# Kernel optimization log

Hardware: AMD Instinct MI355X
Metric: run time of the kernel (lower is better)

The kernel has to match this reference:

```python
import jax, jax.numpy as jnp
import numpy as np

POOLED_H = 7
POOLED_W = 7
SPATIAL_SCALE = 0.0625
B, C, H, W = 8, 256, 48, 48
R = 300
IMG = 768  # = H / SPATIAL_SCALE


def setup_inputs() -> dict:
    key = jax.random.key(0)
    k1, k2, k3, k4 = jax.random.split(key, 4)
    features = jax.random.normal(k1, (B, C, H, W), dtype=jnp.float32)
    # rois: (batch_idx, x1, y1, x2, y2) in input-image coords
    bidx = jax.random.randint(k2, (R, 1), 0, B).astype(jnp.float32)
    tl = jax.random.uniform(k3, (R, 2), minval=0.0, maxval=IMG - 64.0)
    wh = jax.random.uniform(k4, (R, 2), minval=32.0, maxval=320.0)
    br = jnp.minimum(tl + wh, IMG - 1.0)
    rois = jnp.concatenate([bidx, tl, br], axis=1).astype(jnp.float32)
    return {"features": features, "rois": rois}


def _hat_integral(x, grid):
    """Integral from -inf to x of the unit hat basis function centered at each
    grid point g (support [g-1, g+1], peak 1, total mass 1).
    x: [..., 1-broadcastable], grid: [G] -> returns [..., G]."""
    t = x[..., None] - (grid - 1.0)
    return jnp.where(
        t <= 0.0, 0.0,
        jnp.where(t <= 1.0, 0.5 * t * t,
                  jnp.where(t <= 2.0, 1.0 - 0.5 * (2.0 - t) ** 2, 1.0)))


def reference(features, rois):
    # Precise RoI Pooling: exact double integral of the bilinear interpolant
    # over each bin, divided by bin area. Bilinear interp (with zero padding
    # outside the map, as in the CUDA PrRoIPoolingGetData) is
    #   f(u,v) = sum_{j,i} feat[j,i] * hat_j(v) * hat_i(u)
    # so the bin integral factorizes into per-axis hat-integral weights.
    Bf, Cf, Hf, Wf = features.shape
    bidx = rois[:, 0].astype(jnp.int32)
    x1 = rois[:, 1] * SPATIAL_SCALE
    y1 = rois[:, 2] * SPATIAL_SCALE
    x2 = rois[:, 3] * SPATIAL_SCALE
    y2 = rois[:, 4] * SPATIAL_SCALE
    roi_w = jnp.maximum(x2 - x1, 0.0)
    roi_h = jnp.maximum(y2 - y1, 0.0)
    bin_w = roi_w / POOLED_W  # [R]
    bin_h = roi_h / POOLED_H

    ph = jnp.arange(POOLED_H, dtype=jnp.float32)
    pw = jnp.arange(POOLED_W, dtype=jnp.float32)
    ya = y1[:, None] + ph[None, :] * bin_h[:, None]  # [R, PH]
    yb = ya + bin_h[:, None]
    xa = x1[:, None] + pw[None, :] * bin_w[:, None]  # [R, PW]
    xb = xa + bin_w[:, None]

    gy = jnp.arange(Hf, dtype=jnp.float32)
    gx = jnp.arange(Wf, dtype=jnp.float32)
    Wy = _hat_integral(yb, gy) - _hat_integral(ya, gy)  # [R, PH, H]
    Wx = _hat_integral(xb, gx) - _hat_integral(xa, gx)  # [R, PW, W]

    feat = features[bidx]  # [R, C, H, W]
    t = jnp.einsum('rpj,rcji->rcpi', Wy, feat)   # integrate over y
    num = jnp.einsum('rqi,rcpi->rcpq', Wx, t)    # integrate over x -> [R,C,PH,PW]

    area = (bin_w * bin_h)[:, None, None, None]  # win_size per ROI
    out = jnp.where(area > 0.0, num / jnp.where(area > 0.0, area, 1.0), 0.0)
    return out
```

## Files before the change

kernel.cpp:

```cpp
#include <hip/hip_runtime.h>


#define PH 7
#define PW 7
#define NBINS 49
#define SCALE 0.0625f
#define CH 256
#define FH 48
#define FW 48
#define RNUM 300
#define CB 8
#define MAXJ 23
#define ROWF 28

__device__ __forceinline__ float hat_int(float x, float g) {
    float t = x - (g - 1.0f);
    if (t <= 0.0f) return 0.0f;
    if (t <= 1.0f) return 0.5f * t * t;
    if (t <= 2.0f) { float u = 2.0f - t; return 1.0f - 0.5f * u * u; }
    return 1.0f;
}

__global__ __launch_bounds__(256)
void prroi_fused(const float* __restrict__ feat,
                 const float* __restrict__ rois,
                 float* __restrict__ out) {
    const int cblk = blockIdx.x;
    const int r    = blockIdx.y;
    const int c0   = cblk * CB;
    const int tid  = threadIdx.x;

    __shared__ float patch[CB * MAXJ * ROWF];
    __shared__ float s_wy[PH][6];
    __shared__ float s_wx[PW][6];
    __shared__ int   s_jb[PH], s_jc[PH];
    __shared__ int   s_ib[PW], s_ic[PW];

    const float* roi = rois + r * 5;
    const int   b  = (int)roi[0];
    const float x1 = roi[1] * SCALE, y1 = roi[2] * SCALE;
    const float x2 = roi[3] * SCALE, y2 = roi[4] * SCALE;
    const float roi_w = fmaxf(x2 - x1, 0.0f), roi_h = fmaxf(y2 - y1, 0.0f);
    const float bin_w = roi_w / (float)PW, bin_h = roi_h / (float)PH;
    const float area = bin_w * bin_h;
    const float inv_area = (area > 0.0f) ? (1.0f / area) : 0.0f;

    const float ylo = fminf(y1, y2), yhi = fmaxf(y1, y2);
    const float xlo = fminf(x1, x2), xhi = fmaxf(x1, x2);
    const int j0  = max(0, (int)floorf(ylo) - 1);
    const int j1  = min(FH - 1, (int)floorf(yhi) + 1);
    const int i0  = max(0, (int)floorf(xlo) - 1);
    const int i1  = min(FW - 1, (int)floorf(xhi) + 1);
    const int i0a = i0 & ~3;
    const int jspan = j1 - j0 + 1;
    const int ni4   = ((i1 - i0a) >> 2) + 1;

    if (tid < PH + PW) {
        if (tid < PH) {
            const int ph = tid;
            const float ya = y1 + ph * bin_h, yb = ya + bin_h;
            int jb0 = max(0, (int)floorf(ya) - 1);
            int jb1 = min(FH - 1, (int)floorf(yb) + 1);
            jb0 = max(jb0, j0); jb1 = min(jb1, j1);
            s_jb[ph] = jb0 - j0;
            s_jc[ph] = jb1 - jb0 + 1;
#pragma unroll
            for (int k = 0; k < 6; ++k) {
                const float g = (float)(jb0 + k);
                s_wy[ph][k] = hat_int(yb, g) - hat_int(ya, g);
            }
        } else {
            const int pw = tid - PH;
            const float xa = x1 + pw * bin_w, xb = xa + bin_w;
            int ib0 = max(0, (int)floorf(xa) - 1);
            int ib1 = min(FW - 1, (int)floorf(xb) + 1);
            ib0 = max(ib0, i0); ib1 = min(ib1, i1);
            s_ib[pw] = ib0 - i0a;
            s_ic[pw] = ib1 - ib0 + 1;
#pragma unroll
            for (int k = 0; k < 6; ++k) {
                const float g = (float)(ib0 + k);
                s_wx[pw][k] = hat_int(xb, g) - hat_int(xa, g);
            }
        }
    }

    const int per_c  = jspan * ni4;
    const int total  = CB * per_c;
    const float* fb  = feat + (size_t)(b * CH + c0) * FH * FW;
    for (int idx = tid; idx < total; idx += 256) {
        const int c  = idx / per_c;
        const int rj = idx - c * per_c;
        const int j  = rj / ni4;
        const int i4 = rj - j * ni4;
        const float4 v = *(const float4*)(fb + ((size_t)c * FH + (j0 + j)) * FW + i0a + 4 * i4);
        *(float4*)(&patch[(c * MAXJ + j) * ROWF + 4 * i4]) = v;
    }
    __syncthreads();

    const int lane = tid & 63;
    const int wv   = tid >> 6;
    if (lane < NBINS) {
        const int ph = lane / PW;
        const int pw = lane - ph * PW;
        const int jb = s_jb[ph], jc = s_jc[ph];
        const int ib = s_ib[pw], ic = s_ic[pw];
#pragma unroll
        for (int p = 0; p < 2; ++p) {
            const int c = p * 4 + wv;
            const float* pc = &patch[(c * MAXJ + jb) * ROWF + ib];
            float acc = 0.0f;
            for (int jj = 0; jj < jc; ++jj) {
                const float wy = s_wy[ph][jj];
                const float* prow = pc + jj * ROWF;
                float rs = 0.0f;
                for (int ii = 0; ii < ic; ++ii)
                    rs += s_wx[pw][ii] * prow[ii];
                acc += wy * rs;
            }
            out[((size_t)r * CH + c0 + c) * NBINS + lane] = acc * inv_area;
        }
    }
}

extern "C" void kernel_launch(void* const* d_in, const int* in_sizes, int n_in,
                              void* d_out, int out_size, void* d_ws, size_t ws_size,
                              hipStream_t stream) {
    const float* feat = (const float*)d_in[0];
    const float* rois = (const float*)d_in[1];
    float* out = (float*)d_out;

    prroi_fused<<<dim3(CH / CB, RNUM), 256, 0, stream>>>(feat, rois, out);
}
```

Before: 106.3 us.

## Transpose patch to channel-innermost layout and vectorize bin accumulation over channels

Doubles channels per block to 16 and stores the shared-memory patch with channels innermost, transposing four channels at a time during the load. Each thread now handles one bin and four channels, reading float4 across channels and holding the y/x weights in registers, with the inner x loop unrolled. This cuts shared-memory load instructions and weight reloads and halves the block count. The cost is a larger shared footprint, which may lower occupancy, and more lanes left idle (196 of 256 active).

Result: faster. 99.14 us (-6.7%).

```diff
diff --git a/kernel.cpp b/kernel.cpp
--- a/kernel.cpp
+++ b/kernel.cpp
@@ -9,7 +9,7 @@
 #define FH 48
 #define FW 48
 #define RNUM 300
-#define CB 8
+#define CB 16
 #define MAXJ 23
 #define ROWF 28
 
@@ -30,7 +30,7 @@
     const int c0   = cblk * CB;
     const int tid  = threadIdx.x;
 
-    __shared__ float patch[CB * MAXJ * ROWF];
+    __shared__ float patch[MAXJ * ROWF * CB];
     __shared__ float s_wy[PH][6];
     __shared__ float s_wx[PW][6];
     __shared__ int   s_jb[PH], s_jc[PH];
@@ -85,41 +85,62 @@
         }
     }
 
-    const int per_c  = jspan * ni4;
-    const int total  = CB * per_c;
-    const float* fb  = feat + (size_t)(b * CH + c0) * FH * FW;
-    for (int idx = tid; idx < total; idx += 256) {
-        const int c  = idx / per_c;
-        const int rj = idx - c * per_c;
-        const int j  = rj / ni4;
-        const int i4 = rj - j * ni4;
-        const float4 v = *(const float4*)(fb + ((size_t)c * FH + (j0 + j)) * FW + i0a + 4 * i4);
-        *(float4*)(&patch[(c * MAXJ + j) * ROWF + 4 * i4]) = v;
+    const float* fb = feat + (size_t)(b * CH + c0) * FH * FW;
+    for (int u = tid; u < 4 * MAXJ * 7; u += 256) {
+        const int q   = u / (MAXJ * 7);
+        const int rem = u - q * (MAXJ * 7);
+        const int j   = rem / 7;
+        const int i4  = rem - j * 7;
+        if (j < jspan && i4 < ni4) {
+            int ig = i0a + 4 * i4;
+            if (ig > FW - 4) ig = FW - 4;
+            const float* src = fb + ((size_t)(4 * q) * FH + (j0 + j)) * FW + ig;
+            const float4 v0 = *(const float4*)(src);
+            const float4 v1 = *(const float4*)(src + FH * FW);
+            const float4 v2 = *(const float4*)(src + 2 * FH * FW);
+            const float4 v3 = *(const float4*)(src + 3 * FH * FW);
+            float* dst = &patch[((size_t)j * ROWF + (ig - i0a)) * CB + 4 * q];
+            *(float4*)(dst + 0 * CB) = make_float4(v0.x, v1.x, v2.x, v3.x);
+            *(float4*)(dst + 1 * CB) = make_float4(v0.y, v1.y, v2.y, v3.y);
+            *(float4*)(dst + 2 * CB) = make_float4(v0.z, v1.z, v2.z, v3.z);
+            *(float4*)(dst + 3 * CB) = make_float4(v0.w, v1.w, v2.w, v3.w);
+        }
     }
     __syncthreads();
 
-    const int lane = tid & 63;
-    const int wv   = tid >> 6;
-    if (lane < NBINS) {
-        const int ph = lane / PW;
-        const int pw = lane - ph * PW;
+    const int bin = tid >> 2;
+    const int q   = tid & 3;
+    if (bin < NBINS) {
+        const int ph = bin / PW;
+        const int pw = bin - ph * PW;
         const int jb = s_jb[ph], jc = s_jc[ph];
         const int ib = s_ib[pw], ic = s_ic[pw];
+        float wy[6], wx[6];
 #pragma unroll
-        for (int p = 0; p < 2; ++p) {
-            const int c = p * 4 + wv;
-            const float* pc = &patch[(c * MAXJ + jb) * ROWF + ib];
-            float acc = 0.0f;
-            for (int jj = 0; jj < jc; ++jj) {
-                const float wy = s_wy[ph][jj];
-                const float* prow = pc + jj * ROWF;
-                float rs = 0.0f;
-                for (int ii = 0; ii < ic; ++ii)
-                    rs += s_wx[pw][ii] * prow[ii];
-                acc += wy * rs;
+        for (int k = 0; k < 6; ++k) { wy[k] = s_wy[ph][k]; wx[k] = s_wx[pw][k]; }
+
+        float ax = 0.0f, ay = 0.0f, az = 0.0f, aw = 0.0f;
+        const float* pc = &patch[((size_t)jb * ROWF + ib) * CB + 4 * q];
+        for (int jj = 0; jj < jc; ++jj) {
+            const float* prow = pc + (size_t)jj * (ROWF * CB);
+            const float wyj = wy[jj];
+#pragma unroll
+            for (int ii = 0; ii < 6; ++ii) {
+                if (ii < ic) {
+                    const float w = wyj * wx[ii];
+                    const float4 v = *(const float4*)(prow + ii * CB);
+                    ax += w * v.x;
+                    ay += w * v.y;
+                    az += w * v.z;
+                    aw += w * v.w;
+                }
             }
-            out[((size_t)r * CH + c0 + c) * NBINS + lane] = acc * inv_area;
         }
+        float* o = out + ((size_t)r * CH + c0 + 4 * q) * NBINS + bin;
+        o[0 * NBINS] = ax * inv_area;
+        o[1 * NBINS] = ay * inv_area;
+        o[2 * NBINS] = az * inv_area;
+        o[3 * NBINS] = aw * inv_area;
     }
 }
 
```
